# Optimization experiments

Measured on AMD Instinct MI355X. Metric: run time of the kernel, lower is better.

The kernel has to match this reference:

```python
import jax, jax.numpy as jnp
import numpy as np

NEG_SLOPE = 0.2
EPS = 1e-16  # PyG softmax denominator epsilon


def _add_self_loops(src, dst, edge_attr, n):
    # PyG add_self_loops with fill_value='mean': loop edge_attr = mean of
    # incoming edge_attr per target node (0 if no incoming edges).
    cnt = jax.ops.segment_sum(jnp.ones(dst.shape, edge_attr.dtype), dst, n)
    mean_attr = jax.ops.segment_sum(edge_attr, dst, n) / jnp.maximum(cnt, 1.0)[:, None]
    loop = jnp.arange(n)
    return (jnp.concatenate([src, loop]),
            jnp.concatenate([dst, loop]),
            jnp.concatenate([edge_attr, mean_attr], axis=0))


def _gatv2(x, src, dst, eattr, Wl, bl, Wr, br, We, att, bc, n):
    # heads=1, concat=False
    xl = x @ Wl + bl                     # [N, H] source transform
    xr = x @ Wr + br                     # [N, H] target transform
    ee = eattr @ We                      # [E, H]
    m = jax.nn.leaky_relu(xl[src] + xr[dst] + ee, NEG_SLOPE)  # [E, H]
    e = m @ att                          # [E]
    emax = jax.ops.segment_max(e, dst, n)
    emax = jnp.where(jnp.isfinite(emax), emax, 0.0)
    a = jnp.exp(e - emax[dst])
    denom = jax.ops.segment_sum(a, dst, n)
    alpha = a / (denom[dst] + EPS)       # softmax over incoming edges
    out = jax.ops.segment_sum(alpha[:, None] * xl[src], dst, n)  # [N, H]
    return out + bc


def setup_inputs() -> dict:
    key = jax.random.key(0)
    N, E, F_IN, H, E_DIM, OUT = 100000, 1200000, 64, 64, 16, 1
    ks = jax.random.split(key, 20)
    d = {}
    d['x'] = jax.random.normal(ks[0], (N, F_IN), jnp.float32)
    d['edge_index'] = jax.random.randint(ks[1], (2, E), 0, N, jnp.int64)
    d['edge_attr'] = jax.random.normal(ks[2], (E, E_DIM), jnp.float32)
    d['batch'] = jnp.zeros((N,), jnp.int64)
    s = 0.1
    # layer 1: in=F_IN -> H
    d['Wl1'] = jax.random.normal(ks[3], (F_IN, H), jnp.float32) * s
    d['bl1'] = jnp.zeros((H,), jnp.float32)
    d['Wr1'] = jax.random.normal(ks[4], (F_IN, H), jnp.float32) * s
    d['br1'] = jnp.zeros((H,), jnp.float32)
    d['We1'] = jax.random.normal(ks[5], (E_DIM, H), jnp.float32) * s
    d['att1'] = jax.random.normal(ks[6], (H,), jnp.float32) * s
    d['bc1'] = jnp.zeros((H,), jnp.float32)
    # layer 2: H -> H
    d['Wl2'] = jax.random.normal(ks[7], (H, H), jnp.float32) * s
    d['bl2'] = jnp.zeros((H,), jnp.float32)
    d['Wr2'] = jax.random.normal(ks[8], (H, H), jnp.float32) * s
    d['br2'] = jnp.zeros((H,), jnp.float32)
    d['We2'] = jax.random.normal(ks[9], (E_DIM, H), jnp.float32) * s
    d['att2'] = jax.random.normal(ks[10], (H,), jnp.float32) * s
    d['bc2'] = jnp.zeros((H,), jnp.float32)
    # JK(cat) readout: 2*H -> OUT
    d['Wout'] = jax.random.normal(ks[11], (2 * H, OUT), jnp.float32) * s
    d['bout'] = jnp.zeros((OUT,), jnp.float32)
    return d


def reference(x, edge_index, edge_attr, batch,
              Wl1, bl1, Wr1, br1, We1, att1, bc1,
              Wl2, bl2, Wr2, br2, We2, att2, bc2,
              Wout, bout):
    n = x.shape[0]
    src, dst, ea = _add_self_loops(edge_index[0], edge_index[1], edge_attr, n)
    # eval mode: dropout is identity; batch_norms is None
    h1 = jax.nn.relu(_gatv2(x, src, dst, ea, Wl1, bl1, Wr1, br1, We1, att1, bc1, n))
    h2 = jax.nn.relu(_gatv2(h1, src, dst, ea, Wl2, bl2, Wr2, br2, We2, att2, bc2, n))
    h = jnp.concatenate([h1, h2], axis=-1)  # JumpingKnowledge 'cat'
    return h @ Wout + bout                   # [N, out_channels]
```

## Files before the change

kernel.cpp:

```cpp
#include <hip/hip_runtime.h>

constexpr float NEG_SLOPE = 0.2f;
constexpr float EPS = 1e-16f;
constexpr float NEG_INF = -1e30f;

__device__ __forceinline__ unsigned short f2bf(float x) {
    unsigned u = __float_as_uint(x);
    u += 0x7FFF + ((u >> 16) & 1);
    return (unsigned short)(u >> 16);
}
__device__ __forceinline__ float bflo(unsigned u) {
    return __uint_as_float(u << 16);
}
__device__ __forceinline__ float bfhi(unsigned u) {
    return __uint_as_float(u & 0xFFFF0000u);
}
__device__ __forceinline__ unsigned packbf(float a, float b) {
    return (unsigned)f2bf(a) | ((unsigned)f2bf(b) << 16);
}
__device__ __forceinline__ void unpack8(uint4 u, float* o) {
    o[0] = bflo(u.x); o[1] = bfhi(u.x);
    o[2] = bflo(u.y); o[3] = bfhi(u.y);
    o[4] = bflo(u.z); o[5] = bfhi(u.z);
    o[6] = bflo(u.w); o[7] = bfhi(u.w);
}


__global__ void count_k(const int* __restrict__ dst, int* __restrict__ cnt, int E) {
    int i = blockIdx.x * blockDim.x + threadIdx.x;
    if (i < E) atomicAdd(&cnt[dst[i]], 1);
}

__global__ void scan1_k(const int* __restrict__ in, int* __restrict__ out,
                        int* __restrict__ bsum, int n) {
    __shared__ int s[256];
    int tid = threadIdx.x;
    int i = blockIdx.x * 256 + tid;
    int v = (i < n) ? in[i] + 1 : 0;
    s[tid] = v;
    __syncthreads();
    #pragma unroll
    for (int off = 1; off < 256; off <<= 1) {
        int t = (tid >= off) ? s[tid - off] : 0;
        __syncthreads();
        s[tid] += t;
        __syncthreads();
    }
    if (i < n) out[i] = s[tid] - v;
    if (tid == 255) bsum[blockIdx.x] = s[255];
}

__global__ void scan2_k(int* __restrict__ bsum, int nb) {
    __shared__ int s[1024];
    int tid = threadIdx.x;
    int v = (tid < nb) ? bsum[tid] : 0;
    s[tid] = v;
    __syncthreads();
    #pragma unroll
    for (int off = 1; off < 1024; off <<= 1) {
        int t = (tid >= off) ? s[tid - off] : 0;
        __syncthreads();
        s[tid] += t;
        __syncthreads();
    }
    if (tid < nb) bsum[tid] = s[tid] - v;
}

__global__ void scan3_k(int* __restrict__ rowptr, const int* __restrict__ bsum,
                        int n, int M) {
    int i = blockIdx.x * 256 + threadIdx.x;
    if (i < n) rowptr[i] += bsum[blockIdx.x];
    if (i == 0) rowptr[n] = M;
}

__global__ void fill_k(const int* __restrict__ dst,
                       const int* __restrict__ rowptr, int* __restrict__ fill,
                       int* __restrict__ seid, int E) {
    int i = blockIdx.x * blockDim.x + threadIdx.x;
    if (i < E) {
        int d = dst[i];
        int pos = rowptr[d] + atomicAdd(&fill[d], 1);
        seid[pos] = i;
    }
}

__global__ void expand_k(const int* __restrict__ rowptr, int* __restrict__ sdst, int N) {
    int lane = threadIdx.x & 63;
    int v = blockIdx.x * 4 + (threadIdx.x >> 6);
    if (v >= N) return;
    int s = rowptr[v], e = rowptr[v + 1];
    for (int k = s + lane; k < e; k += 64) sdst[k] = v;
}

template <int PERM>
__global__ void build_k(const int* __restrict__ srcA, const float* __restrict__ ea,
                        const int* __restrict__ seid,
                        int* __restrict__ ssrc, unsigned short* __restrict__ eperm_b,
                        int M) {
    int t = blockIdx.x * blockDim.x + threadIdx.x;
    if (t >= M * 2) return;
    int k = t >> 1, c = t & 1;
    int eid = seid[k];
    if (eid < 0) return;
    if (c == 0) ssrc[k] = srcA[eid];
    if (PERM) {
        const float4* s4 = reinterpret_cast<const float4*>(ea) + (size_t)eid * 4 + c * 2;
        float4 a = s4[0], b = s4[1];
        uint4 o;
        o.x = packbf(a.x, a.y);
        o.y = packbf(a.z, a.w);
        o.z = packbf(b.x, b.y);
        o.w = packbf(b.z, b.w);
        reinterpret_cast<uint4*>(eperm_b)[(size_t)k * 2 + c] = o;
    }
}

template <int PERM>
__global__ void mean_k(const float* __restrict__ ea, const int* __restrict__ seid,
                       const int* __restrict__ rowptr,
                       unsigned short* __restrict__ eperm_b, float* __restrict__ mattr,
                       int* __restrict__ ssrc, int N) {
    int t = blockIdx.x * blockDim.x + threadIdx.x;
    if (t >= N * 16) return;
    int v = t >> 4, f = t & 15;
    int s = rowptr[v], sEnd = rowptr[v + 1] - 1;
    float sum = 0.f;
    for (int k = s; k < sEnd; k++) {
        if (PERM) sum += bflo((unsigned)eperm_b[(size_t)k * 16 + f]);
        else      sum += ea[(size_t)seid[k] * 16 + f];
    }
    int c = sEnd - s;
    float mean = sum / (float)(c > 1 ? c : 1);
    if (PERM) eperm_b[(size_t)sEnd * 16 + f] = f2bf(mean);
    else      mattr[(size_t)v * 16 + f] = mean;
    if (f == 0) ssrc[sEnd] = v;
}


__global__ __launch_bounds__(256) void xfrm_k(
        const float* __restrict__ x,
        const float* __restrict__ Wl, const float* __restrict__ bl,
        const float* __restrict__ Wr, const float* __restrict__ br,
        unsigned short* __restrict__ xl_b, unsigned short* __restrict__ xr_b, int N) {
    __shared__ float2 sW[64 * 64];
    for (int i = threadIdx.x; i < 64 * 64; i += 256)
        sW[i] = make_float2(Wl[i], Wr[i]);
    __syncthreads();

    int lane = threadIdx.x & 63;
    int base = __builtin_amdgcn_readfirstlane(
        (blockIdx.x * 4 + (threadIdx.x >> 6)) * 8);
    if (base >= N) return;

    const float4* xb = reinterpret_cast<const float4*>(x);
    int r[8];
    #pragma unroll
    for (int n = 0; n < 8; ++n) r[n] = min(base + n, N - 1) * 16;

    float blh = bl[lane], brh = br[lane];
    float2 acc[8];
    #pragma unroll
    for (int n = 0; n < 8; ++n) acc[n] = make_float2(blh, brh);

    #pragma unroll 4
    for (int d4 = 0; d4 < 16; ++d4) {
        float4 xv[8];
        #pragma unroll
        for (int n = 0; n < 8; ++n) xv[n] = xb[r[n] + d4];
        #pragma unroll
        for (int j = 0; j < 4; ++j) {
            float2 wp = sW[(d4 * 4 + j) * 64 + lane];
            #pragma unroll
            for (int n = 0; n < 8; ++n) {
                float xs = (j == 0) ? xv[n].x : (j == 1) ? xv[n].y
                         : (j == 2) ? xv[n].z : xv[n].w;
                acc[n].x = fmaf(xs, wp.x, acc[n].x);
                acc[n].y = fmaf(xs, wp.y, acc[n].y);
            }
        }
    }

    #pragma unroll
    for (int n = 0; n < 8; ++n) {
        int v = base + n;
        if (v < N) {
            xl_b[(size_t)v * 64 + lane] = f2bf(acc[n].x);
            xr_b[(size_t)v * 64 + lane] = f2bf(acc[n].y);
        }
    }
}


template <int PERM>
__global__ __launch_bounds__(256) void escore_k(
        const unsigned short* __restrict__ xl_b, const unsigned short* __restrict__ xr_b,
        const unsigned short* __restrict__ eperm_b,
        const float* __restrict__ earaw, const int* __restrict__ seid,
        const float* __restrict__ mattr,
        const int* __restrict__ ssrc, const int* __restrict__ sdst,
        const float* __restrict__ We, const float* __restrict__ att,
        float* __restrict__ escr, int M) {
    __shared__ float4 sWe[16 * 16];
    __shared__ float4 sAtt[16];
    int tid = threadIdx.x;
    {
        const float4* We4 = reinterpret_cast<const float4*>(We);
        if (tid < 256) sWe[tid] = We4[tid];
        if (tid < 16) sAtt[tid] = reinterpret_cast<const float4*>(att)[tid];
    }
    __syncthreads();

    int lane = tid & 63;
    int base = (blockIdx.x * 4 + (tid >> 6)) * 128;
    if (base >= M) return;
    int k0 = base + lane;
    int k1 = k0 + 64;
    int k0c = min(k0, M - 1);
    int k1c = min(k1, M - 1);

    int s0 = ssrc[k0c], d0 = sdst[k0c];
    int s1 = ssrc[k1c], d1 = sdst[k1c];

    float ea0[16], ea1[16];
    if (PERM) {
        const uint4* ep4 = reinterpret_cast<const uint4*>(eperm_b);
        uint4 a0 = ep4[(size_t)k0c * 2], a1 = ep4[(size_t)k0c * 2 + 1];
        uint4 b0 = ep4[(size_t)k1c * 2], b1 = ep4[(size_t)k1c * 2 + 1];
        unpack8(a0, ea0); unpack8(a1, ea0 + 8);
        unpack8(b0, ea1); unpack8(b1, ea1 + 8);
    } else {
        int e0 = seid[k0c], e1 = seid[k1c];
        const float4* rp0 = (e0 < 0)
            ? reinterpret_cast<const float4*>(mattr) + (size_t)d0 * 4
            : reinterpret_cast<const float4*>(earaw) + (size_t)e0 * 4;
        const float4* rp1 = (e1 < 0)
            ? reinterpret_cast<const float4*>(mattr) + (size_t)d1 * 4
            : reinterpret_cast<const float4*>(earaw) + (size_t)e1 * 4;
        #pragma unroll
        for (int q = 0; q < 4; q++) {
            float4 a = rp0[q];
            ea0[q * 4 + 0] = a.x; ea0[q * 4 + 1] = a.y;
            ea0[q * 4 + 2] = a.z; ea0[q * 4 + 3] = a.w;
            float4 b = rp1[q];
            ea1[q * 4 + 0] = b.x; ea1[q * 4 + 1] = b.y;
            ea1[q * 4 + 2] = b.z; ea1[q * 4 + 3] = b.w;
        }
    }

    const uint2* xl2 = reinterpret_cast<const uint2*>(xl_b);
    const uint2* xr2 = reinterpret_cast<const uint2*>(xr_b);
    size_t xs0 = (size_t)s0 * 16, xd0 = (size_t)d0 * 16;
    size_t xs1 = (size_t)s1 * 16, xd1 = (size_t)d1 * 16;

    float acc0 = 0.f, acc1 = 0.f;
    #pragma unroll 4
    for (int j = 0; j < 16; ++j) {
        uint2 ux0 = xl2[xs0 + j];
        uint2 ur0 = xr2[xd0 + j];
        uint2 ux1 = xl2[xs1 + j];
        uint2 ur1 = xr2[xd1 + j];
        float4 ee0 = {0.f, 0.f, 0.f, 0.f};
        float4 ee1 = {0.f, 0.f, 0.f, 0.f};
        #pragma unroll
        for (int d = 0; d < 16; ++d) {
            float4 w = sWe[d * 16 + j];
            float a0 = ea0[d], a1 = ea1[d];
            ee0.x = fmaf(a0, w.x, ee0.x);
            ee0.y = fmaf(a0, w.y, ee0.y);
            ee0.z = fmaf(a0, w.z, ee0.z);
            ee0.w = fmaf(a0, w.w, ee0.w);
            ee1.x = fmaf(a1, w.x, ee1.x);
            ee1.y = fmaf(a1, w.y, ee1.y);
            ee1.z = fmaf(a1, w.z, ee1.z);
            ee1.w = fmaf(a1, w.w, ee1.w);
        }
        float4 a4 = sAtt[j];
        float m;
        m = bflo(ux0.x) + bflo(ur0.x) + ee0.x; m = (m > 0.f) ? m : NEG_SLOPE * m; acc0 = fmaf(a4.x, m, acc0);
        m = bfhi(ux0.x) + bfhi(ur0.x) + ee0.y; m = (m > 0.f) ? m : NEG_SLOPE * m; acc0 = fmaf(a4.y, m, acc0);
        m = bflo(ux0.y) + bflo(ur0.y) + ee0.z; m = (m > 0.f) ? m : NEG_SLOPE * m; acc0 = fmaf(a4.z, m, acc0);
        m = bfhi(ux0.y) + bfhi(ur0.y) + ee0.w; m = (m > 0.f) ? m : NEG_SLOPE * m; acc0 = fmaf(a4.w, m, acc0);
        m = bflo(ux1.x) + bflo(ur1.x) + ee1.x; m = (m > 0.f) ? m : NEG_SLOPE * m; acc1 = fmaf(a4.x, m, acc1);
        m = bfhi(ux1.x) + bfhi(ur1.x) + ee1.y; m = (m > 0.f) ? m : NEG_SLOPE * m; acc1 = fmaf(a4.y, m, acc1);
        m = bflo(ux1.y) + bflo(ur1.y) + ee1.z; m = (m > 0.f) ? m : NEG_SLOPE * m; acc1 = fmaf(a4.z, m, acc1);
        m = bfhi(ux1.y) + bfhi(ur1.y) + ee1.w; m = (m > 0.f) ? m : NEG_SLOPE * m; acc1 = fmaf(a4.w, m, acc1);
    }
    if (k0 < M) escr[k0] = acc0;
    if (k1 < M) escr[k1] = acc1;
}


__device__ __forceinline__ float rdlanef(float x, int j) {
    return __int_as_float(__builtin_amdgcn_readlane(__float_as_int(x), j));
}

template <int MODE>
__global__ __launch_bounds__(256) void aggregate_k(
        const unsigned short* __restrict__ xl_b, const float* __restrict__ escr,
        const int* __restrict__ ssrc, const int* __restrict__ rowptr,
        const float* __restrict__ bc,
        float* __restrict__ hout,
        const float* __restrict__ h1, const float* __restrict__ Wout,
        const float* __restrict__ bout, float* __restrict__ out, int N) {
    int lane = threadIdx.x & 63;
    int v = blockIdx.x * 4 + (threadIdx.x >> 6);
    if (v >= N) return;

    int s = rowptr[v], e = rowptr[v + 1];
    int deg = e - s;
    float acc;

    if (deg <= 64) {
        int idx = s + lane;
        bool valid = lane < deg;
        float sc = valid ? escr[idx] : NEG_INF;
        float m = sc;
        #pragma unroll
        for (int off = 32; off; off >>= 1) m = fmaxf(m, __shfl_xor(m, off));
        float t = valid ? __expf(sc - m) : 0.f;
        float dsum = t;
        #pragma unroll
        for (int off = 32; off; off >>= 1) dsum += __shfl_xor(dsum, off);
        float alpha = t / (dsum + EPS);
        int srcn = valid ? ssrc[idx] : 0;

        float a0 = 0.f, a1 = 0.f, a2 = 0.f, a3 = 0.f;
        int j = 0;
        for (; j + 4 <= deg; j += 4) {
            int sj0 = __builtin_amdgcn_readlane(srcn, j);
            int sj1 = __builtin_amdgcn_readlane(srcn, j + 1);
            int sj2 = __builtin_amdgcn_readlane(srcn, j + 2);
            int sj3 = __builtin_amdgcn_readlane(srcn, j + 3);
            float w0 = rdlanef(alpha, j);
            float w1 = rdlanef(alpha, j + 1);
            float w2 = rdlanef(alpha, j + 2);
            float w3 = rdlanef(alpha, j + 3);
            a0 = fmaf(w0, bflo((unsigned)xl_b[(size_t)sj0 * 64 + lane]), a0);
            a1 = fmaf(w1, bflo((unsigned)xl_b[(size_t)sj1 * 64 + lane]), a1);
            a2 = fmaf(w2, bflo((unsigned)xl_b[(size_t)sj2 * 64 + lane]), a2);
            a3 = fmaf(w3, bflo((unsigned)xl_b[(size_t)sj3 * 64 + lane]), a3);
        }
        for (; j < deg; ++j) {
            int sj = __builtin_amdgcn_readlane(srcn, j);
            float wj = rdlanef(alpha, j);
            a0 = fmaf(wj, bflo((unsigned)xl_b[(size_t)sj * 64 + lane]), a0);
        }
        acc = (a0 + a1) + (a2 + a3);
    } else {
        float m = NEG_INF;
        for (int b = s; b < e; b += 64) {
            int idx = b + lane;
            float val = (idx < e) ? escr[idx] : NEG_INF;
            #pragma unroll
            for (int off = 32; off; off >>= 1) val = fmaxf(val, __shfl_xor(val, off));
            m = fmaxf(m, val);
        }
        float denom = 0.f;
        for (int b = s; b < e; b += 64) {
            int idx = b + lane;
            float t = (idx < e) ? __expf(escr[idx] - m) : 0.f;
            #pragma unroll
            for (int off = 32; off; off >>= 1) t += __shfl_xor(t, off);
            denom += t;
        }
        float inv = 1.f / (denom + EPS);
        acc = 0.f;
        for (int b = s; b < e; b += 64) {
            int idx = b + lane;
            float wv = (idx < e) ? __expf(escr[idx] - m) * inv : 0.f;
            int srcn = (idx < e) ? ssrc[idx] : 0;
            int nj = min(64, e - b);
            for (int j = 0; j < nj; ++j) {
                float wk = rdlanef(wv, j);
                int sj = __builtin_amdgcn_readlane(srcn, j);
                acc = fmaf(wk, bflo((unsigned)xl_b[(size_t)sj * 64 + lane]), acc);
            }
        }
    }

    float res = fmaxf(acc + bc[lane], 0.f);

    if (MODE == 0) {
        hout[(size_t)v * 64 + lane] = res;
    } else {
        float part = h1[(size_t)v * 64 + lane] * Wout[lane] + res * Wout[64 + lane];
        #pragma unroll
        for (int off = 32; off; off >>= 1) part += __shfl_xor(part, off);
        if (lane == 0) out[v] = part + bout[0];
    }
}


extern "C" void kernel_launch(void* const* d_in, const int* in_sizes, int n_in,
                              void* d_out, int out_size, void* d_ws, size_t ws_size,
                              hipStream_t stream) {
    const float* x     = (const float*)d_in[0];
    const int*   eidx  = (const int*)d_in[1];
    const float* eattr = (const float*)d_in[2];
    const float* Wl1 = (const float*)d_in[4];
    const float* bl1 = (const float*)d_in[5];
    const float* Wr1 = (const float*)d_in[6];
    const float* br1 = (const float*)d_in[7];
    const float* We1 = (const float*)d_in[8];
    const float* att1 = (const float*)d_in[9];
    const float* bc1 = (const float*)d_in[10];
    const float* Wl2 = (const float*)d_in[11];
    const float* bl2 = (const float*)d_in[12];
    const float* Wr2 = (const float*)d_in[13];
    const float* br2 = (const float*)d_in[14];
    const float* We2 = (const float*)d_in[15];
    const float* att2 = (const float*)d_in[16];
    const float* bc2 = (const float*)d_in[17];
    const float* Wout = (const float*)d_in[18];
    const float* bout = (const float*)d_in[19];

    int N = in_sizes[0] / 64;
    int E = in_sizes[1] / 2;
    int M = E + N;
    const int* srcA = eidx;
    const int* dstA = eidx + E;

    char* w = (char*)d_ws;
    size_t used = 0;
    auto alloc = [&](size_t bytes) {
        char* p = w + used;
        used += (bytes + 255) & ~size_t(255);
        return p;
    };
    int*   cnt    = (int*)alloc((size_t)N * 4);
    int*   fill   = (int*)alloc((size_t)N * 4);
    int*   rowptr = (int*)alloc((size_t)(N + 1) * 4);
    int*   bsum   = (int*)alloc(1024 * 4);
    int*   ssrc   = (int*)alloc((size_t)M * 4);
    int*   sdst   = (int*)alloc((size_t)M * 4);
    int*   seid   = (int*)alloc((size_t)M * 4);
    float* escr   = (float*)alloc((size_t)M * 4);
    float* mattr  = (float*)alloc((size_t)N * 16 * 4);
    unsigned short* xl_b = (unsigned short*)alloc((size_t)N * 64 * 2);
    unsigned short* xr_b = (unsigned short*)alloc((size_t)N * 64 * 2);
    float* h1     = (float*)alloc((size_t)N * 64 * 4);
    size_t eperm_bytes = (size_t)M * 16 * 2;
    bool perm = (used + eperm_bytes) <= ws_size;
    unsigned short* eperm_b = perm ? (unsigned short*)alloc(eperm_bytes) : nullptr;

    hipMemsetAsync(cnt, 0, (size_t)N * 4, stream);
    hipMemsetAsync(fill, 0, (size_t)N * 4, stream);
    hipMemsetAsync(seid, 0xFF, (size_t)M * 4, stream);

    int NB = (N + 255) / 256;
    int nodeBlocks = (N + 3) / 4;
    count_k<<<(E + 255) / 256, 256, 0, stream>>>(dstA, cnt, E);
    scan1_k<<<NB, 256, 0, stream>>>(cnt, rowptr, bsum, N);
    scan2_k<<<1, 1024, 0, stream>>>(bsum, NB);
    scan3_k<<<NB, 256, 0, stream>>>(rowptr, bsum, N, M);
    fill_k<<<(E + 255) / 256, 256, 0, stream>>>(dstA, rowptr, fill, seid, E);
    expand_k<<<nodeBlocks, 256, 0, stream>>>(rowptr, sdst, N);

    if (perm) {
        build_k<1><<<(M * 2 + 255) / 256, 256, 0, stream>>>(srcA, eattr, seid,
                                                            ssrc, eperm_b, M);
        mean_k<1><<<(N * 16 + 255) / 256, 256, 0, stream>>>(
            eattr, seid, rowptr, eperm_b, mattr, ssrc, N);
    } else {
        build_k<0><<<(M * 2 + 255) / 256, 256, 0, stream>>>(srcA, eattr, seid,
                                                            ssrc, nullptr, M);
        mean_k<0><<<(N * 16 + 255) / 256, 256, 0, stream>>>(
            eattr, seid, rowptr, nullptr, mattr, ssrc, N);
    }

    int xfrmBlocks = (N + 31) / 32;
    int slotBlocks = (M + 511) / 512;

    xfrm_k<<<xfrmBlocks, 256, 0, stream>>>(x, Wl1, bl1, Wr1, br1, xl_b, xr_b, N);
    if (perm)
        escore_k<1><<<slotBlocks, 256, 0, stream>>>(xl_b, xr_b, eperm_b, eattr, seid,
                                                    mattr, ssrc, sdst, We1, att1, escr, M);
    else
        escore_k<0><<<slotBlocks, 256, 0, stream>>>(xl_b, xr_b, nullptr, eattr, seid,
                                                    mattr, ssrc, sdst, We1, att1, escr, M);
    aggregate_k<0><<<nodeBlocks, 256, 0, stream>>>(xl_b, escr, ssrc, rowptr, bc1, h1,
                                                   nullptr, nullptr, nullptr, nullptr, N);

    xfrm_k<<<xfrmBlocks, 256, 0, stream>>>(h1, Wl2, bl2, Wr2, br2, xl_b, xr_b, N);
    if (perm)
        escore_k<1><<<slotBlocks, 256, 0, stream>>>(xl_b, xr_b, eperm_b, eattr, seid,
                                                    mattr, ssrc, sdst, We2, att2, escr, M);
    else
        escore_k<0><<<slotBlocks, 256, 0, stream>>>(xl_b, xr_b, nullptr, eattr, seid,
                                                    mattr, ssrc, sdst, We2, att2, escr, M);
    aggregate_k<1><<<nodeBlocks, 256, 0, stream>>>(xl_b, escr, ssrc, rowptr, bc2, nullptr,
                                                   h1, Wout, bout, (float*)d_out, N);
}
```

Before: 533.0 us.

## Pack sorted src and edge id into int2, store h1 as bf16

The fill kernel now writes (src, edge id) pairs into one interleaved int2 array during the CSR scatter. This removes the separate build pass that gathered src through the edge id, and lets consumers read src and id in one load. Layer-1 output h1 is stored in bf16, halving its write and read traffic in the second transform and the readout. The cost is a wider 8-byte entry wherever only src is needed, and extra bf16 rounding on h1 that could shift accuracy.

```diff
diff --git a/kernel.cpp b/kernel.cpp
--- a/kernel.cpp
+++ b/kernel.cpp
@@ -73,14 +73,14 @@
     if (i == 0) rowptr[n] = M;
 }
 
-__global__ void fill_k(const int* __restrict__ dst,
-                       const int* __restrict__ rowptr, int* __restrict__ fill,
-                       int* __restrict__ seid, int E) {
+__global__ void fill_k(const int* __restrict__ src, const int* __restrict__ dst,
+                       const int* __restrict__ rowptr, int* __restrict__ fillc,
+                       int2* __restrict__ sedge, int E) {
     int i = blockIdx.x * blockDim.x + threadIdx.x;
     if (i < E) {
         int d = dst[i];
-        int pos = rowptr[d] + atomicAdd(&fill[d], 1);
-        seid[pos] = i;
+        int pos = rowptr[d] + atomicAdd(&fillc[d], 1);
+        sedge[pos] = make_int2(src[i], i);
     }
 }
 
@@ -92,34 +92,28 @@
     for (int k = s + lane; k < e; k += 64) sdst[k] = v;
 }
 
-template <int PERM>
-__global__ void build_k(const int* __restrict__ srcA, const float* __restrict__ ea,
-                        const int* __restrict__ seid,
-                        int* __restrict__ ssrc, unsigned short* __restrict__ eperm_b,
-                        int M) {
+__global__ void permute_k(const float* __restrict__ ea, const int2* __restrict__ sedge,
+                          unsigned short* __restrict__ eperm_b, int M) {
     int t = blockIdx.x * blockDim.x + threadIdx.x;
     if (t >= M * 2) return;
     int k = t >> 1, c = t & 1;
-    int eid = seid[k];
+    int eid = sedge[k].y;
     if (eid < 0) return;
-    if (c == 0) ssrc[k] = srcA[eid];
-    if (PERM) {
-        const float4* s4 = reinterpret_cast<const float4*>(ea) + (size_t)eid * 4 + c * 2;
-        float4 a = s4[0], b = s4[1];
-        uint4 o;
-        o.x = packbf(a.x, a.y);
-        o.y = packbf(a.z, a.w);
-        o.z = packbf(b.x, b.y);
-        o.w = packbf(b.z, b.w);
-        reinterpret_cast<uint4*>(eperm_b)[(size_t)k * 2 + c] = o;
-    }
+    const float4* s4 = reinterpret_cast<const float4*>(ea) + (size_t)eid * 4 + c * 2;
+    float4 a = s4[0], b = s4[1];
+    uint4 o;
+    o.x = packbf(a.x, a.y);
+    o.y = packbf(a.z, a.w);
+    o.z = packbf(b.x, b.y);
+    o.w = packbf(b.z, b.w);
+    reinterpret_cast<uint4*>(eperm_b)[(size_t)k * 2 + c] = o;
 }
 
 template <int PERM>
-__global__ void mean_k(const float* __restrict__ ea, const int* __restrict__ seid,
+__global__ void mean_k(const float* __restrict__ ea, const int2* __restrict__ sedge_c,
                        const int* __restrict__ rowptr,
                        unsigned short* __restrict__ eperm_b, float* __restrict__ mattr,
-                       int* __restrict__ ssrc, int N) {
+                       int2* __restrict__ sedge, int N) {
     int t = blockIdx.x * blockDim.x + threadIdx.x;
     if (t >= N * 16) return;
     int v = t >> 4, f = t & 15;
@@ -127,18 +121,19 @@
     float sum = 0.f;
     for (int k = s; k < sEnd; k++) {
         if (PERM) sum += bflo((unsigned)eperm_b[(size_t)k * 16 + f]);
-        else      sum += ea[(size_t)seid[k] * 16 + f];
+        else      sum += ea[(size_t)sedge_c[k].y * 16 + f];
     }
     int c = sEnd - s;
     float mean = sum / (float)(c > 1 ? c : 1);
     if (PERM) eperm_b[(size_t)sEnd * 16 + f] = f2bf(mean);
     else      mattr[(size_t)v * 16 + f] = mean;
-    if (f == 0) ssrc[sEnd] = v;
-}
-
-
+    if (f == 0) sedge[sEnd] = make_int2(v, -1);
+}
+
+
+template <int BF>
 __global__ __launch_bounds__(256) void xfrm_k(
-        const float* __restrict__ x,
+        const float* __restrict__ xf, const unsigned short* __restrict__ xb16,
         const float* __restrict__ Wl, const float* __restrict__ bl,
         const float* __restrict__ Wr, const float* __restrict__ br,
         unsigned short* __restrict__ xl_b, unsigned short* __restrict__ xr_b, int N) {
@@ -152,7 +147,8 @@
         (blockIdx.x * 4 + (threadIdx.x >> 6)) * 8);
     if (base >= N) return;
 
-    const float4* xb = reinterpret_cast<const float4*>(x);
+    const float4* xb = reinterpret_cast<const float4*>(xf);
+    const uint2*  xh = reinterpret_cast<const uint2*>(xb16);
     int r[8];
     #pragma unroll
     for (int n = 0; n < 8; ++n) r[n] = min(base + n, N - 1) * 16;
@@ -166,7 +162,14 @@
     for (int d4 = 0; d4 < 16; ++d4) {
         float4 xv[8];
         #pragma unroll
-        for (int n = 0; n < 8; ++n) xv[n] = xb[r[n] + d4];
+        for (int n = 0; n < 8; ++n) {
+            if (BF) {
+                uint2 u = xh[r[n] + d4];
+                xv[n] = make_float4(bflo(u.x), bfhi(u.x), bflo(u.y), bfhi(u.y));
+            } else {
+                xv[n] = xb[r[n] + d4];
+            }
+        }
         #pragma unroll
         for (int j = 0; j < 4; ++j) {
             float2 wp = sW[(d4 * 4 + j) * 64 + lane];
@@ -195,9 +198,8 @@
 __global__ __launch_bounds__(256) void escore_k(
         const unsigned short* __restrict__ xl_b, const unsigned short* __restrict__ xr_b,
         const unsigned short* __restrict__ eperm_b,
-        const float* __restrict__ earaw, const int* __restrict__ seid,
-        const float* __restrict__ mattr,
-        const int* __restrict__ ssrc, const int* __restrict__ sdst,
+        const float* __restrict__ earaw, const int2* __restrict__ sedge,
+        const float* __restrict__ mattr, const int* __restrict__ sdst,
         const float* __restrict__ We, const float* __restrict__ att,
         float* __restrict__ escr, int M) {
     __shared__ float4 sWe[16 * 16];
@@ -218,8 +220,9 @@
     int k0c = min(k0, M - 1);
     int k1c = min(k1, M - 1);
 
-    int s0 = ssrc[k0c], d0 = sdst[k0c];
-    int s1 = ssrc[k1c], d1 = sdst[k1c];
+    int2 se0 = sedge[k0c], se1 = sedge[k1c];
+    int s0 = se0.x, s1 = se1.x;
+    int d0 = sdst[k0c], d1 = sdst[k1c];
 
     float ea0[16], ea1[16];
     if (PERM) {
@@ -229,7 +232,7 @@
         unpack8(a0, ea0); unpack8(a1, ea0 + 8);
         unpack8(b0, ea1); unpack8(b1, ea1 + 8);
     } else {
-        int e0 = seid[k0c], e1 = seid[k1c];
+        int e0 = se0.y, e1 = se1.y;
         const float4* rp0 = (e0 < 0)
             ? reinterpret_cast<const float4*>(mattr) + (size_t)d0 * 4
             : reinterpret_cast<const float4*>(earaw) + (size_t)e0 * 4;
@@ -297,10 +300,10 @@
 template <int MODE>
 __global__ __launch_bounds__(256) void aggregate_k(
         const unsigned short* __restrict__ xl_b, const float* __restrict__ escr,
-        const int* __restrict__ ssrc, const int* __restrict__ rowptr,
+        const int2* __restrict__ sedge, const int* __restrict__ rowptr,
         const float* __restrict__ bc,
-        float* __restrict__ hout,
-        const float* __restrict__ h1, const float* __restrict__ Wout,
+        unsigned short* __restrict__ hout_b,
+        const unsigned short* __restrict__ h1_b, const float* __restrict__ Wout,
         const float* __restrict__ bout, float* __restrict__ out, int N) {
     int lane = threadIdx.x & 63;
     int v = blockIdx.x * 4 + (threadIdx.x >> 6);
@@ -322,7 +325,7 @@
         #pragma unroll
         for (int off = 32; off; off >>= 1) dsum += __shfl_xor(dsum, off);
         float alpha = t / (dsum + EPS);
-        int srcn = valid ? ssrc[idx] : 0;
+        int srcn = valid ? sedge[idx].x : 0;
 
         float a0 = 0.f, a1 = 0.f, a2 = 0.f, a3 = 0.f;
         int j = 0;
@@ -368,7 +371,7 @@
         for (int b = s; b < e; b += 64) {
             int idx = b + lane;
             float wv = (idx < e) ? __expf(escr[idx] - m) * inv : 0.f;
-            int srcn = (idx < e) ? ssrc[idx] : 0;
+            int srcn = (idx < e) ? sedge[idx].x : 0;
             int nj = min(64, e - b);
             for (int j = 0; j < nj; ++j) {
                 float wk = rdlanef(wv, j);
@@ -381,9 +384,10 @@
     float res = fmaxf(acc + bc[lane], 0.f);
 
     if (MODE == 0) {
-        hout[(size_t)v * 64 + lane] = res;
+        hout_b[(size_t)v * 64 + lane] = f2bf(res);
     } else {
-        float part = h1[(size_t)v * 64 + lane] * Wout[lane] + res * Wout[64 + lane];
+        float part = bflo((unsigned)h1_b[(size_t)v * 64 + lane]) * Wout[lane]
+                   + res * Wout[64 + lane];
         #pragma unroll
         for (int off = 32; off; off >>= 1) part += __shfl_xor(part, off);
         if (lane == 0) out[v] = part + bout[0];
@@ -428,24 +432,23 @@
         return p;
     };
     int*   cnt    = (int*)alloc((size_t)N * 4);
-    int*   fill   = (int*)alloc((size_t)N * 4);
+    int*   fillc  = (int*)alloc((size_t)N * 4);
     int*   rowptr = (int*)alloc((size_t)(N + 1) * 4);
     int*   bsum   = (int*)alloc(1024 * 4);
-    int*   ssrc   = (int*)alloc((size_t)M * 4);
+    int2*  sedge  = (int2*)alloc((size_t)M * 8);
     int*   sdst   = (int*)alloc((size_t)M * 4);
-    int*   seid   = (int*)alloc((size_t)M * 4);
     float* escr   = (float*)alloc((size_t)M * 4);
     float* mattr  = (float*)alloc((size_t)N * 16 * 4);
     unsigned short* xl_b = (unsigned short*)alloc((size_t)N * 64 * 2);
     unsigned short* xr_b = (unsigned short*)alloc((size_t)N * 64 * 2);
-    float* h1     = (float*)alloc((size_t)N * 64 * 4);
+    unsigned short* h1_b = (unsigned short*)alloc((size_t)N * 64 * 2);
     size_t eperm_bytes = (size_t)M * 16 * 2;
     bool perm = (used + eperm_bytes) <= ws_size;
     unsigned short* eperm_b = perm ? (unsigned short*)alloc(eperm_bytes) : nullptr;
 
     hipMemsetAsync(cnt, 0, (size_t)N * 4, stream);
-    hipMemsetAsync(fill, 0, (size_t)N * 4, stream);
-    hipMemsetAsync(seid, 0xFF, (size_t)M * 4, stream);
+    hipMemsetAsync(fillc, 0, (size_t)N * 4, stream);
+    hipMemsetAsync(sedge, 0xFF, (size_t)M * 8, stream);
 
     int NB = (N + 255) / 256;
     int nodeBlocks = (N + 3) / 4;
@@ -453,41 +456,40 @@
     scan1_k<<<NB, 256, 0, stream>>>(cnt, rowptr, bsum, N);
     scan2_k<<<1, 1024, 0, stream>>>(bsum, NB);
     scan3_k<<<NB, 256, 0, stream>>>(rowptr, bsum, N, M);
-    fill_k<<<(E + 255) / 256, 256, 0, stream>>>(dstA, rowptr, fill, seid, E);
+    fill_k<<<(E + 255) / 256, 256, 0, stream>>>(srcA, dstA, rowptr, fillc, sedge, E);
     expand_k<<<nodeBlocks, 256, 0, stream>>>(rowptr, sdst, N);
 
     if (perm) {
-        build_k<1><<<(M * 2 + 255) / 256, 256, 0, stream>>>(srcA, eattr, seid,
-                                                            ssrc, eperm_b, M);
+        permute_k<<<(M * 2 + 255) / 256, 256, 0, stream>>>(eattr, sedge, eperm_b, M);
         mean_k<1><<<(N * 16 + 255) / 256, 256, 0, stream>>>(
-            eattr, seid, rowptr, eperm_b, mattr, ssrc, N);
+            eattr, sedge, rowptr, eperm_b, mattr, sedge, N);
     } else {
-        build_k<0><<<(M * 2 + 255) / 256, 256, 0, stream>>>(srcA, eattr, seid,
-                                                            ssrc, nullptr, M);
         mean_k<0><<<(N * 16 + 255) / 256, 256, 0, stream>>>(
-            eattr, seid, rowptr, nullptr, mattr, ssrc, N);
+            eattr, sedge, rowptr, nullptr, mattr, sedge, N);
     }
 
     int xfrmBlocks = (N + 31) / 32;
     int slotBlocks = (M + 511) / 512;
 
-    xfrm_k<<<xfrmBlocks, 256, 0, stream>>>(x, Wl1, bl1, Wr1, br1, xl_b, xr_b, N);
+    xfrm_k<0><<<xfrmBlocks, 256, 0, stream>>>(x, nullptr, Wl1, bl1, Wr1, br1,
+                                              xl_b, xr_b, N);
     if (perm)
-        escore_k<1><<<slotBlocks, 256, 0, stream>>>(xl_b, xr_b, eperm_b, eattr, seid,
-                                                    mattr, ssrc, sdst, We1, att1, escr, M);
+        escore_k<1><<<slotBlocks, 256, 0, stream>>>(xl_b, xr_b, eperm_b, eattr, sedge,
+                                                    mattr, sdst, We1, att1, escr, M);
     else
-        escore_k<0><<<slotBlocks, 256, 0, stream>>>(xl_b, xr_b, nullptr, eattr, seid,
-                                                    mattr, ssrc, sdst, We1, att1, escr, M);
-    aggregate_k<0><<<nodeBlocks, 256, 0, stream>>>(xl_b, escr, ssrc, rowptr, bc1, h1,
+        escore_k<0><<<slotBlocks, 256, 0, stream>>>(xl_b, xr_b, nullptr, eattr, sedge,
+                                                    mattr, sdst, We1, att1, escr, M);
+    aggregate_k<0><<<nodeBlocks, 256, 0, stream>>>(xl_b, escr, sedge, rowptr, bc1, h1_b,
                                                    nullptr, nullptr, nullptr, nullptr, N);
 
-    xfrm_k<<<xfrmBlocks, 256, 0, stream>>>(h1, Wl2, bl2, Wr2, br2, xl_b, xr_b, N);
+    xfrm_k<1><<<xfrmBlocks, 256, 0, stream>>>(nullptr, h1_b, Wl2, bl2, Wr2, br2,
+                                              xl_b, xr_b, N);
     if (perm)
-        escore_k<1><<<slotBlocks, 256, 0, stream>>>(xl_b, xr_b, eperm_b, eattr, seid,
-                                                    mattr, ssrc, sdst, We2, att2, escr, M);
+        escore_k<1><<<slotBlocks, 256, 0, stream>>>(xl_b, xr_b, eperm_b, eattr, sedge,
+                                                    mattr, sdst, We2, att2, escr, M);
     else
-        escore_k<0><<<slotBlocks, 256, 0, stream>>>(xl_b, xr_b, nullptr, eattr, seid,
-                                                    mattr, ssrc, sdst, We2, att2, escr, M);
-    aggregate_k<1><<<nodeBlocks, 256, 0, stream>>>(xl_b, escr, ssrc, rowptr, bc2, nullptr,
-                                                   h1, Wout, bout, (float*)d_out, N);
-}
+        escore_k<0><<<slotBlocks, 256, 0, stream>>>(xl_b, xr_b, nullptr, eattr, sedge,
+                                                    mattr, sdst, We2, att2, escr, M);
+    aggregate_k<1><<<nodeBlocks, 256, 0, stream>>>(xl_b, escr, sedge, rowptr, bc2, nullptr,
+                                                   h1_b, Wout, bout, (float*)d_out, N);
+}
```

Measured after the change: 554.6 us. 1.04x slower.
